# Kernel tuning notes

Measured on AMD Instinct MI355X. Metric: run time of the kernel, lower is better.

Reference implementation:

```python
import jax, jax.numpy as jnp
import numpy as np

HID = 1152      # vision_hidden_size
HEADS = 16      # vision_num_heads
HD = HID // HEADS  # 72
INTER = 4304    # vision_intermediate_size
SEQ = 16384     # total vision tokens
WIN = 64        # tokens per attention window
EPS = 1e-6


def setup_inputs() -> dict:
    key = jax.random.key(0)
    ks = jax.random.split(key, 14)
    f32 = jnp.float32
    x = jax.random.normal(ks[0], (SEQ, HID), f32)
    # RoPE tables: standard rotary angles, full head_dim via concat(ang, ang)
    inv_freq = 1.0 / (10000.0 ** (jnp.arange(0, HD // 2, dtype=f32) / (HD // 2)))
    ang = jnp.arange(SEQ, dtype=f32)[:, None] * inv_freq[None, :]
    emb = jnp.concatenate([ang, ang], axis=-1)          # [SEQ, HD]
    cos, sin = jnp.cos(emb), jnp.sin(emb)
    cu_seqlens = jnp.arange(SEQ // WIN + 1, dtype=jnp.int32) * WIN  # uniform windows
    sc = 0.02
    return {
        "x": x, "cos": cos, "sin": sin, "cu_seqlens": cu_seqlens,
        "qkv_w": jax.random.normal(ks[1], (HID, 3 * HID), f32) * sc,
        "qkv_b": jnp.zeros((3 * HID,), f32),
        "proj_w": jax.random.normal(ks[2], (HID, HID), f32) * sc,
        "proj_b": jnp.zeros((HID,), f32),
        "ln1_w": jnp.ones((HID,), f32), "ln1_b": jnp.zeros((HID,), f32),
        "ln2_w": jnp.ones((HID,), f32), "ln2_b": jnp.zeros((HID,), f32),
        "fc1_w": jax.random.normal(ks[3], (HID, INTER), f32) * sc,
        "fc1_b": jnp.zeros((INTER,), f32),
        "fc2_w": jax.random.normal(ks[4], (INTER, HID), f32) * sc,
        "fc2_b": jnp.zeros((HID,), f32),
    }


def _layer_norm(h, w, b):
    hf = h.astype(jnp.float32)
    mean = jnp.mean(hf, axis=-1, keepdims=True)
    var = jnp.mean((hf - mean) ** 2, axis=-1, keepdims=True)
    return ((hf - mean) * jax.lax.rsqrt(var + EPS)) * w + b


def _rotate_half(t):
    t1, t2 = jnp.split(t, 2, axis=-1)
    return jnp.concatenate((-t2, t1), axis=-1)


def reference(x, cos, sin, cu_seqlens,
              qkv_w, qkv_b, proj_w, proj_b,
              ln1_w, ln1_b, ln2_w, ln2_b,
              fc1_w, fc1_b, fc2_w, fc2_b):
    S = x.shape[0]
    n_win = cu_seqlens.shape[0] - 1
    W = S // n_win  # uniform windows (block-diagonal attention)

    # --- attention branch ---
    h = _layer_norm(x, ln1_w, ln1_b)
    qkv = h @ qkv_w + qkv_b
    q, k, v = jnp.split(qkv, 3, axis=-1)
    q = q.reshape(S, HEADS, HD)
    k = k.reshape(S, HEADS, HD)
    v = v.reshape(S, HEADS, HD)
    c = cos[:, None, :HD]
    s = sin[:, None, :HD]
    q = q * c + _rotate_half(q) * s
    k = k * c + _rotate_half(k) * s
    # block-diagonal windowed attention: [n_win, W, HEADS, HD]
    qw = q.reshape(n_win, W, HEADS, HD).astype(jnp.float32)
    kw = k.reshape(n_win, W, HEADS, HD).astype(jnp.float32)
    vw = v.reshape(n_win, W, HEADS, HD).astype(jnp.float32)
    scores = jnp.einsum('wqhd,wkhd->whqk', qw, kw) * (HD ** -0.5)
    probs = jax.nn.softmax(scores, axis=-1)
    out = jnp.einsum('whqk,wkhd->wqhd', probs, vw).reshape(S, HID)
    x = x + (out @ proj_w + proj_b)

    # --- MLP branch ---
    h2 = _layer_norm(x, ln2_w, ln2_b)
    m = jax.nn.gelu(h2 @ fc1_w + fc1_b, approximate=True)
    return x + (m @ fc2_w + fc2_b)
```

## Files before the change

### kernel.cpp

```cpp
#include <hip/hip_runtime.h>
#include <stdint.h>


#define SEQ   16384
#define HID   1152
#define NH    16
#define HDIM  72
#define INTER 4304
#define INTERP 4352
#define QKVN  3456

using bf16x8 = __attribute__((ext_vector_type(8))) __bf16;
using f32x4  = __attribute__((ext_vector_type(4))) float;

__device__ __forceinline__ float bf2f(uint16_t u){ return __uint_as_float(((uint32_t)u)<<16); }
__device__ __forceinline__ uint16_t f2bf(float f){
  uint32_t u = __float_as_uint(f);
  u += 0x7fffu + ((u>>16)&1u);
  return (uint16_t)(u>>16);
}
__device__ __forceinline__ float gelu_tanh(float x){
  float t = tanhf(0.7978845608028654f*(x + 0.044715f*x*x*x));
  return 0.5f*x*(1.0f + t);
}
__device__ __forceinline__ void async_load16(const void* g, void* l){
  __builtin_amdgcn_global_load_lds((__attribute__((address_space(1))) void*)(void*)g,
                                   (__attribute__((address_space(3))) void*)l, 16, 0, 0);
}

__global__ void transpose_cast(const float* __restrict__ src, uint16_t* __restrict__ dst,
                               int R, int C, int Rp)
{
  __shared__ float tile[32][33];
  const int tx = threadIdx.x & 31, ty = threadIdx.x >> 5;
  const int c = blockIdx.x*32 + tx;
  #pragma unroll
  for (int s = 0; s < 4; ++s){
    const int r = blockIdx.y*32 + ty + s*8;
    tile[ty + s*8][tx] = (r < R && c < C) ? src[(size_t)r*C + c] : 0.0f;
  }
  __syncthreads();
  #pragma unroll
  for (int s = 0; s < 4; ++s){
    const int oc = blockIdx.x*32 + ty + s*8;
    const int orr = blockIdx.y*32 + tx;
    dst[(size_t)oc*Rp + orr] = f2bf(tile[tx][ty + s*8]);
  }
}

__global__ void ln_kernel(const float* __restrict__ x, const float* __restrict__ w,
                          const float* __restrict__ b, uint16_t* __restrict__ out)
{
  const int wid = threadIdx.x >> 6, lane = threadIdx.x & 63;
  const int row = blockIdx.x*4 + wid;
  const float* xr = x + (size_t)row*HID;
  float v[18];
  float s = 0.f;
  #pragma unroll
  for (int t = 0; t < 18; ++t){ v[t] = xr[lane + t*64]; s += v[t]; }
  #pragma unroll
  for (int m = 32; m; m >>= 1) s += __shfl_xor(s, m, 64);
  const float mean = s * (1.0f/HID);
  float q = 0.f;
  #pragma unroll
  for (int t = 0; t < 18; ++t){ float d = v[t]-mean; q += d*d; }
  #pragma unroll
  for (int m = 32; m; m >>= 1) q += __shfl_xor(q, m, 64);
  const float rstd = rsqrtf(q*(1.0f/HID) + 1e-6f);
  uint16_t* orow = out + (size_t)row*HID;
  #pragma unroll
  for (int t = 0; t < 18; ++t){
    const int j = lane + t*64;
    orow[j] = f2bf((v[t]-mean)*rstd*w[j] + b[j]);
  }
}

__global__ void rope_kernel(uint16_t* __restrict__ qkv, const float* __restrict__ cosb,
                            const float* __restrict__ sinb)
{
  const int idx = blockIdx.x*256 + threadIdx.x;
  const int s  = idx / (NH*36);
  const int r1 = idx - s*(NH*36);
  const int h  = r1 / 36;
  const int d  = r1 - h*36;
  const float c  = cosb[s*HDIM + d];
  const float sn = sinb[s*HDIM + d];
  const size_t b = (size_t)s*QKVN + h*HDIM + d;
  float q1 = bf2f(qkv[b]), q2 = bf2f(qkv[b+36]);
  qkv[b]    = f2bf(q1*c - q2*sn);
  qkv[b+36] = f2bf(q2*c + q1*sn);
  float k1 = bf2f(qkv[b+HID]), k2 = bf2f(qkv[b+HID+36]);
  qkv[b+HID]    = f2bf(k1*c - k2*sn);
  qkv[b+HID+36] = f2bf(k2*c + k1*sn);
}

__global__ __launch_bounds__(256,2) void attn_kernel(const uint16_t* __restrict__ qkv,
                                                     uint16_t* __restrict__ outb)
{
  __shared__ float Q[64*76];
  __shared__ float K[64*76];
  __shared__ float V[64*76];
  __shared__ float P[64*68];
  const int tid = threadIdx.x;
  const int win = blockIdx.x >> 4, h = blockIdx.x & 15;
  const size_t base = (size_t)win*64*QKVN + h*HDIM;
  {
    const int r = tid >> 2, q4 = tid & 3;
    const size_t rb = base + (size_t)r*QKVN;
    #pragma unroll
    for (int p0 = 0; p0 < 9; ++p0){
      const int p = q4*9 + p0;
      const uint32_t uq = *(const uint32_t*)(qkv + rb + 2*p);
      const uint32_t uk = *(const uint32_t*)(qkv + rb + HID + 2*p);
      const uint32_t uv = *(const uint32_t*)(qkv + rb + 2*HID + 2*p);
      Q[r*76+2*p] = bf2f((uint16_t)uq); Q[r*76+2*p+1] = bf2f((uint16_t)(uq>>16));
      K[r*76+2*p] = bf2f((uint16_t)uk); K[r*76+2*p+1] = bf2f((uint16_t)(uk>>16));
      V[r*76+2*p] = bf2f((uint16_t)uv); V[r*76+2*p+1] = bf2f((uint16_t)(uv>>16));
    }
  }
  __syncthreads();
  const int rg = tid >> 4, cg = tid & 15;
  const int r0 = rg*4, c0 = cg*4;
  float sc[4][4] = {};
  #pragma unroll 3
  for (int kk = 0; kk < 18; ++kk){
    float4 qv[4], kv[4];
    #pragma unroll
    for (int i = 0; i < 4; ++i) qv[i] = *(const float4*)&Q[(r0+i)*76 + kk*4];
    #pragma unroll
    for (int j = 0; j < 4; ++j) kv[j] = *(const float4*)&K[(c0+j)*76 + kk*4];
    #pragma unroll
    for (int i = 0; i < 4; ++i)
      #pragma unroll
      for (int j = 0; j < 4; ++j)
        sc[i][j] += qv[i].x*kv[j].x + qv[i].y*kv[j].y + qv[i].z*kv[j].z + qv[i].w*kv[j].w;
  }
  const float scale = 0.11785113019775793f;
  #pragma unroll
  for (int i = 0; i < 4; ++i){
    float a0 = sc[i][0]*scale, a1 = sc[i][1]*scale, a2 = sc[i][2]*scale, a3 = sc[i][3]*scale;
    float m = fmaxf(fmaxf(a0,a1), fmaxf(a2,a3));
    m = fmaxf(m, __shfl_xor(m, 1, 16));
    m = fmaxf(m, __shfl_xor(m, 2, 16));
    m = fmaxf(m, __shfl_xor(m, 4, 16));
    m = fmaxf(m, __shfl_xor(m, 8, 16));
    float e0 = __expf(a0-m), e1 = __expf(a1-m), e2 = __expf(a2-m), e3 = __expf(a3-m);
    float sm = e0+e1+e2+e3;
    sm += __shfl_xor(sm, 1, 16);
    sm += __shfl_xor(sm, 2, 16);
    sm += __shfl_xor(sm, 4, 16);
    sm += __shfl_xor(sm, 8, 16);
    const float inv = 1.0f/sm;
    *(float4*)&P[(r0+i)*68 + c0] = make_float4(e0*inv, e1*inv, e2*inv, e3*inv);
  }
  __syncthreads();
  for (int d4 = cg; d4 < 18; d4 += 16){
    float4 o[4] = {};
    #pragma unroll 4
    for (int k4 = 0; k4 < 16; ++k4){
      float4 pr[4];
      #pragma unroll
      for (int i = 0; i < 4; ++i) pr[i] = *(const float4*)&P[(r0+i)*68 + k4*4];
      const float4 v0 = *(const float4*)&V[(k4*4+0)*76 + d4*4];
      const float4 v1 = *(const float4*)&V[(k4*4+1)*76 + d4*4];
      const float4 v2 = *(const float4*)&V[(k4*4+2)*76 + d4*4];
      const float4 v3 = *(const float4*)&V[(k4*4+3)*76 + d4*4];
      #pragma unroll
      for (int i = 0; i < 4; ++i){
        o[i].x += pr[i].x*v0.x + pr[i].y*v1.x + pr[i].z*v2.x + pr[i].w*v3.x;
        o[i].y += pr[i].x*v0.y + pr[i].y*v1.y + pr[i].z*v2.y + pr[i].w*v3.y;
        o[i].z += pr[i].x*v0.z + pr[i].y*v1.z + pr[i].z*v2.z + pr[i].w*v3.z;
        o[i].w += pr[i].x*v0.w + pr[i].y*v1.w + pr[i].z*v2.w + pr[i].w*v3.w;
      }
    }
    #pragma unroll
    for (int i = 0; i < 4; ++i){
      const int token = win*64 + r0 + i;
      const size_t ob = (size_t)token*HID + h*HDIM + d4*4;
      outb[ob+0] = f2bf(o[i].x); outb[ob+1] = f2bf(o[i].y);
      outb[ob+2] = f2bf(o[i].z); outb[ob+3] = f2bf(o[i].w);
    }
  }
}

template<int EPI>
__global__ __launch_bounds__(256,3) void gemm_bt(
    const uint16_t* __restrict__ A, const uint16_t* __restrict__ Bt,
    const float* __restrict__ bias, int Nb,
    const float* res, void* outp, int N, int K, int NB)
{
  __shared__ uint16_t sA[128*64];
  __shared__ uint16_t sB[128*64];
  const int tid = threadIdx.x, wid = tid >> 6, lane = tid & 63;
  const int per  = gridDim.x >> 3;
  const int tile = (blockIdx.x & 7)*per + (blockIdx.x >> 3);
  const int mb   = tile / NB;
  const int mBase = mb*128, nBase = (tile - mb*NB)*128;
  const int wm = wid >> 1, wn = wid & 1;
  const int sr = lane >> 2;
  const int sk = lane & 3;
  const int gk = sk ^ ((sr >> 1) & 3);
  const int rr = lane & 15;
  const int rq = lane >> 4;
  const int rp = rq ^ ((rr >> 1) & 3);
  f32x4 acc[4][4] = {};

  for (int k0 = 0; k0 < K; k0 += 64){
    __syncthreads();
    #pragma unroll
    for (int j = 0; j < 4; ++j){
      const int c  = wid*4 + j;
      const int rc = c >> 1, h = c & 1;
      const size_t gcol = (size_t)(k0 + h*32 + gk*8);
      async_load16(A  + (size_t)(mBase + rc*16 + sr)*K + gcol, &sA[c*512]);
      async_load16(Bt + (size_t)(nBase + rc*16 + sr)*K + gcol, &sB[c*512]);
    }
    __syncthreads();
    #pragma unroll
    for (int h = 0; h < 2; ++h){
      bf16x8 af[4], bfr[4];
      #pragma unroll
      for (int i = 0; i < 4; ++i)
        af[i] = *(const bf16x8*)&sA[((wm*4 + i)*2 + h)*512 + rr*32 + rp*8];
      #pragma unroll
      for (int j = 0; j < 4; ++j)
        bfr[j] = *(const bf16x8*)&sB[((wn*4 + j)*2 + h)*512 + rr*32 + rp*8];
      #pragma unroll
      for (int i = 0; i < 4; ++i)
        #pragma unroll
        for (int j = 0; j < 4; ++j)
          acc[i][j] = __builtin_amdgcn_mfma_f32_16x16x32_bf16(af[i], bfr[j], acc[i][j], 0, 0, 0);
    }
  }

  const int rqd = (lane>>4)*4, cl = lane & 15;
  #pragma unroll
  for (int i = 0; i < 4; ++i){
    #pragma unroll
    for (int j = 0; j < 4; ++j){
      const int col = nBase + wn*64 + j*16 + cl;
      const float bv = (col < Nb) ? bias[col] : 0.0f;
      #pragma unroll
      for (int r = 0; r < 4; ++r){
        const int row = mBase + wm*64 + i*16 + rqd + r;
        const float v = acc[i][j][r] + bv;
        const size_t o = (size_t)row*N + col;
        if (EPI == 0)      ((uint16_t*)outp)[o] = f2bf(v);
        else if (EPI == 1) ((uint16_t*)outp)[o] = f2bf(gelu_tanh(v));
        else               ((float*)outp)[o] = v + res[o];
      }
    }
  }
}

extern "C" void kernel_launch(void* const* d_in, const int* in_sizes, int n_in,
                              void* d_out, int out_size, void* d_ws, size_t ws_size,
                              hipStream_t stream)
{
  const float* x      = (const float*)d_in[0];
  const float* cosb   = (const float*)d_in[1];
  const float* sinb   = (const float*)d_in[2];
  const float* qkv_w  = (const float*)d_in[4];
  const float* qkv_b  = (const float*)d_in[5];
  const float* proj_w = (const float*)d_in[6];
  const float* proj_b = (const float*)d_in[7];
  const float* ln1_w  = (const float*)d_in[8];
  const float* ln1_b  = (const float*)d_in[9];
  const float* ln2_w  = (const float*)d_in[10];
  const float* ln2_b  = (const float*)d_in[11];
  const float* fc1_w  = (const float*)d_in[12];
  const float* fc1_b  = (const float*)d_in[13];
  const float* fc2_w  = (const float*)d_in[14];
  const float* fc2_b  = (const float*)d_in[15];

  char* ws = (char*)d_ws;
  uint16_t* Wqkv  = (uint16_t*)(ws + 0);
  uint16_t* Wproj = (uint16_t*)(ws + 7962624);
  uint16_t* Wfc1  = (uint16_t*)(ws + 10616832);
  uint16_t* Wfc2  = (uint16_t*)(ws + 20643840);
  uint16_t* Hbuf  = (uint16_t*)(ws + 30670848);
  uint16_t* QKV   = (uint16_t*)(ws + 68419584);
  uint16_t* MB    = QKV;
  float* X1 = (float*)d_out;

  transpose_cast<<<dim3(108,36), 256, 0, stream>>>(qkv_w, Wqkv, 1152, 3456, 1152);
  transpose_cast<<<dim3(36,36),  256, 0, stream>>>(proj_w, Wproj, 1152, 1152, 1152);
  transpose_cast<<<dim3(136,36), 256, 0, stream>>>(fc1_w, Wfc1, 1152, 4304, 1152);
  transpose_cast<<<dim3(36,136), 256, 0, stream>>>(fc2_w, Wfc2, 4304, 1152, 4352);

  ln_kernel<<<4096, 256, 0, stream>>>(x, ln1_w, ln1_b, Hbuf);
  gemm_bt<0><<<27*128, 256, 0, stream>>>(Hbuf, Wqkv, qkv_b, QKVN, nullptr, QKV, QKVN, HID, 27);
  rope_kernel<<<36864, 256, 0, stream>>>(QKV, cosb, sinb);
  attn_kernel<<<4096, 256, 0, stream>>>(QKV, Hbuf);
  gemm_bt<2><<<9*128, 256, 0, stream>>>(Hbuf, Wproj, proj_b, HID, x, X1, HID, HID, 9);
  ln_kernel<<<4096, 256, 0, stream>>>(X1, ln2_w, ln2_b, Hbuf);
  gemm_bt<1><<<34*128, 256, 0, stream>>>(Hbuf, Wfc1, fc1_b, INTER, nullptr, MB, INTERP, HID, 34);
  gemm_bt<2><<<9*128, 256, 0, stream>>>(MB, Wfc2, fc2_b, HID, X1, X1, HID, INTERP, 9);
}
```

Measured before the change: 1.180 ms.

## Double-buffer GEMM LDS loads and switch to 32x32x16 MFMA tiles

Rewrites the bf16 GEMM main loop to use a K-step of 32 with two LDS buffers, so the async global-to-LDS loads for the next step are issued before computing the current one. Explicit waitcnt and barriers replace the two __syncthreads per iteration. Each wave now uses 2x2 32x32x16 MFMAs instead of 4x4 16x16x32, with a new XOR swizzle and epilogue mapping. Occupancy target rises to 4 blocks per CU. The shorter K-step means more barriers per K, and the hand-coded waitcnt encodings must match the number of outstanding loads.

```diff
diff --git a/kernel.cpp b/kernel.cpp
--- a/kernel.cpp
+++ b/kernel.cpp
@@ -11,7 +11,7 @@
 #define QKVN  3456
 
 using bf16x8 = __attribute__((ext_vector_type(8))) __bf16;
-using f32x4  = __attribute__((ext_vector_type(4))) float;
+using f32x16 = __attribute__((ext_vector_type(16))) float;
 
 __device__ __forceinline__ float bf2f(uint16_t u){ return __uint_as_float(((uint32_t)u)<<16); }
 __device__ __forceinline__ uint16_t f2bf(float f){
@@ -184,66 +184,86 @@
 }
 
 template<int EPI>
-__global__ __launch_bounds__(256,3) void gemm_bt(
+__global__ __launch_bounds__(256,4) void gemm_bt(
     const uint16_t* __restrict__ A, const uint16_t* __restrict__ Bt,
     const float* __restrict__ bias, int Nb,
     const float* res, void* outp, int N, int K, int NB)
 {
-  __shared__ uint16_t sA[128*64];
-  __shared__ uint16_t sB[128*64];
+  __shared__ uint16_t sm[16384];
   const int tid = threadIdx.x, wid = tid >> 6, lane = tid & 63;
   const int per  = gridDim.x >> 3;
   const int tile = (blockIdx.x & 7)*per + (blockIdx.x >> 3);
   const int mb   = tile / NB;
   const int mBase = mb*128, nBase = (tile - mb*NB)*128;
   const int wm = wid >> 1, wn = wid & 1;
-  const int sr = lane >> 2;
-  const int sk = lane & 3;
-  const int gk = sk ^ ((sr >> 1) & 3);
-  const int rr = lane & 15;
-  const int rq = lane >> 4;
-  const int rp = rq ^ ((rr >> 1) & 3);
-  f32x4 acc[4][4] = {};
-
-  for (int k0 = 0; k0 < K; k0 += 64){
-    __syncthreads();
-    #pragma unroll
-    for (int j = 0; j < 4; ++j){
-      const int c  = wid*4 + j;
-      const int rc = c >> 1, h = c & 1;
-      const size_t gcol = (size_t)(k0 + h*32 + gk*8);
-      async_load16(A  + (size_t)(mBase + rc*16 + sr)*K + gcol, &sA[c*512]);
-      async_load16(Bt + (size_t)(nBase + rc*16 + sr)*K + gcol, &sB[c*512]);
-    }
-    __syncthreads();
-    #pragma unroll
-    for (int h = 0; h < 2; ++h){
-      bf16x8 af[4], bfr[4];
+
+  const int fs0 = wid*128 + lane, fs1 = fs0 + 64;
+  const int r0s = fs0 >> 2, g0 = (fs0 & 3) ^ (r0s & 3);
+  const int r1s = fs1 >> 2, g1 = (fs1 & 3) ^ (r1s & 3);
+  const uint16_t* a0 = A  + (size_t)(mBase + r0s)*K + g0*8;
+  const uint16_t* a1 = A  + (size_t)(mBase + r1s)*K + g1*8;
+  const uint16_t* b0 = Bt + (size_t)(nBase + r0s)*K + g0*8;
+  const uint16_t* b1 = Bt + (size_t)(nBase + r1s)*K + g1*8;
+  uint16_t* ldsA0 = sm + wid*1024;
+  uint16_t* ldsA1 = sm + wid*1024 + 512;
+  uint16_t* ldsB0 = sm + 4096 + wid*1024;
+  uint16_t* ldsB1 = sm + 4096 + wid*1024 + 512;
+
+  const int rl = lane & 31, lh = lane >> 5, lx = lane & 3;
+  int offA[2][2], offB[2][2];
+  #pragma unroll
+  for (int i = 0; i < 2; ++i)
+    #pragma unroll
+    for (int s = 0; s < 2; ++s){
+      offA[i][s] = (wm*64 + i*32 + rl)*32 + (((s*2 + lh) ^ lx) * 8);
+      offB[i][s] = 4096 + (wn*64 + i*32 + rl)*32 + (((s*2 + lh) ^ lx) * 8);
+    }
+
+  f32x16 acc[2][2] = {};
+  const int NI = K >> 5;
+
+  async_load16(a0, ldsA0); async_load16(a1, ldsA1);
+  async_load16(b0, ldsB0); async_load16(b1, ldsB1);
+
+  for (int it = 0; it < NI; ++it){
+    const int cur = it & 1;
+    if (it + 1 < NI){
+      const int k0 = (it + 1) << 5;
+      const int bo = (cur ^ 1) * 8192;
+      async_load16(a0 + k0, ldsA0 + bo); async_load16(a1 + k0, ldsA1 + bo);
+      async_load16(b0 + k0, ldsB0 + bo); async_load16(b1 + k0, ldsB1 + bo);
+      __builtin_amdgcn_s_waitcnt(0x0F74);
+    } else {
+      __builtin_amdgcn_s_waitcnt(0x0F70);
+    }
+    __builtin_amdgcn_s_barrier();
+    __builtin_amdgcn_sched_barrier(0);
+    const uint16_t* smb = sm + cur*8192;
+    #pragma unroll
+    for (int s = 0; s < 2; ++s){
+      bf16x8 af0 = *(const bf16x8*)&smb[offA[0][s]];
+      bf16x8 af1 = *(const bf16x8*)&smb[offA[1][s]];
+      bf16x8 bf0 = *(const bf16x8*)&smb[offB[0][s]];
+      bf16x8 bf1 = *(const bf16x8*)&smb[offB[1][s]];
+      acc[0][0] = __builtin_amdgcn_mfma_f32_32x32x16_bf16(af0, bf0, acc[0][0], 0, 0, 0);
+      acc[0][1] = __builtin_amdgcn_mfma_f32_32x32x16_bf16(af0, bf1, acc[0][1], 0, 0, 0);
+      acc[1][0] = __builtin_amdgcn_mfma_f32_32x32x16_bf16(af1, bf0, acc[1][0], 0, 0, 0);
+      acc[1][1] = __builtin_amdgcn_mfma_f32_32x32x16_bf16(af1, bf1, acc[1][1], 0, 0, 0);
+    }
+    __builtin_amdgcn_sched_barrier(0);
+    __builtin_amdgcn_s_barrier();
+  }
+
+  #pragma unroll
+  for (int j = 0; j < 2; ++j){
+    const int col = nBase + wn*64 + j*32 + rl;
+    const float bv = (col < Nb) ? bias[col] : 0.0f;
+    #pragma unroll
+    for (int i = 0; i < 2; ++i){
       #pragma unroll
-      for (int i = 0; i < 4; ++i)
-        af[i] = *(const bf16x8*)&sA[((wm*4 + i)*2 + h)*512 + rr*32 + rp*8];
-      #pragma unroll
-      for (int j = 0; j < 4; ++j)
-        bfr[j] = *(const bf16x8*)&sB[((wn*4 + j)*2 + h)*512 + rr*32 + rp*8];
-      #pragma unroll
-      for (int i = 0; i < 4; ++i)
-        #pragma unroll
-        for (int j = 0; j < 4; ++j)
-          acc[i][j] = __builtin_amdgcn_mfma_f32_16x16x32_bf16(af[i], bfr[j], acc[i][j], 0, 0, 0);
-    }
-  }
-
-  const int rqd = (lane>>4)*4, cl = lane & 15;
-  #pragma unroll
-  for (int i = 0; i < 4; ++i){
-    #pragma unroll
-    for (int j = 0; j < 4; ++j){
-      const int col = nBase + wn*64 + j*16 + cl;
-      const float bv = (col < Nb) ? bias[col] : 0.0f;
-      #pragma unroll
-      for (int r = 0; r < 4; ++r){
-        const int row = mBase + wm*64 + i*16 + rqd + r;
-        const float v = acc[i][j][r] + bv;
+      for (int reg = 0; reg < 16; ++reg){
+        const int row = mBase + wm*64 + i*32 + (reg & 3) + 8*(reg >> 2) + 4*lh;
+        const float v = acc[i][j][reg] + bv;
         const size_t o = (size_t)row*N + col;
         if (EPI == 0)      ((uint16_t*)outp)[o] = f2bf(v);
         else if (EPI == 1) ((uint16_t*)outp)[o] = f2bf(gelu_tanh(v));
```

Measured after the change: 1.263 ms. 1.07x slower.
